# Kernel tuning notes

Hardware: AMD Instinct MI355X
Metric: run time of the kernel (lower is better)

Reference implementation:

```python
import jax, jax.numpy as jnp
import numpy as np

B, S = 512, 256          # batch, seq_len
C, H = 8, 16             # num_cells, expert hidden size
M = 20                   # memory_size (hard-coded in module)
NT = C * H               # num_trajectories = 128
ENC_IN = M * (NT + 1)    # 20*129 = 2580, memory_encode input dim
A_H = 16                 # agent LSTM hidden


def setup_inputs() -> dict:
    key = jax.random.key(0)
    ks = jax.random.split(key, 20)
    r = lambda i, shape: 0.1 * jax.random.normal(ks[i], shape, dtype=jnp.float32)
    return {
        "x": jax.random.normal(ks[0], (B, S, 1), dtype=jnp.float32),
        "pred0": jax.random.uniform(ks[1], (B, 1), dtype=jnp.float32),
        "gate0": jax.nn.softmax(jax.random.uniform(ks[2], (B, C), dtype=jnp.float32), axis=1),
        # experts: C parallel LSTM cells (input 1, hidden H) + per-cell scalar head
        "W_ih": r(3, (C, 4 * H, 1)), "W_hh": r(4, (C, 4 * H, H)),
        "b_ih": r(5, (C, 4 * H)), "b_hh": r(6, (C, 4 * H)),
        "W_o": r(7, (C, H)), "b_o": r(8, (C,)),
        # memory_encode: Linear(2580,64) ReLU Linear(64,16) ReLU
        "W1": r(9, (64, ENC_IN)), "b1": r(10, (64,)),
        "W2": r(11, (16, 64)), "b2": r(12, (16,)),
        # gate_linear: Linear(16, C) + softmax
        "Wg": r(13, (C, 16)), "bg": r(14, (C,)),
        # agent: 2 stacked LSTM cells (16 -> 16)
        "Wa_ih": r(15, (2, 4 * A_H, A_H)), "Wa_hh": r(16, (2, 4 * A_H, A_H)),
        "ba_ih": r(17, (2, 4 * A_H)), "ba_hh": r(18, (2, 4 * A_H)),
    }


def _cell(z, c):
    # PyTorch LSTMCell gate order: i, f, g, o
    i, f, g, o = jnp.split(z, 4, axis=-1)
    c2 = jax.nn.sigmoid(f) * c + jax.nn.sigmoid(i) * jnp.tanh(g)
    return jax.nn.sigmoid(o) * jnp.tanh(c2), c2


def reference(x, pred0, gate0, W_ih, W_hh, b_ih, b_hh, W_o, b_o,
              W1, b1, W2, b2, Wg, bg, Wa_ih, Wa_hh, ba_ih, ba_hh):
    mem0 = jnp.zeros((B, M, NT + 1), jnp.float32).at[:, :, -1].set(0.5)
    eh0 = jnp.zeros((B, H), jnp.float32)   # combined expert h (shared across cells)
    a0 = jnp.zeros((2, B, A_H), jnp.float32)

    def step(carry, x_t):
        mem, eh, ec, pred, gate_state, ah, ac = carry
        error = x_t - pred                                        # [B,1]
        # experts: C LSTM cells, all reading the shared combined state
        z = (jnp.einsum('bf,cgf->bcg', x_t, W_ih)
             + jnp.einsum('bh,cgh->bcg', eh, W_hh)
             + b_ih + b_hh)                                       # [B,C,4H]
        nh, nc = _cell(z, ec[:, None, :])                          # [B,C,H]
        o = jnp.einsum('bch,ch->bc', nh, W_o) + b_o               # [B,C]
        # memory_step: matmul(mstep, mem) shifts rows down by 1, row 0 <- w
        w = jnp.concatenate([nh.reshape(B, -1), error], axis=1)   # [B,NT+1]
        mem = jnp.concatenate([w[:, None, :], mem[:, :-1, :]], axis=1)
        # memory_encode MLP
        e1 = jax.nn.relu(mem.reshape(B, -1) @ W1.T + b1)
        ai = jax.nn.relu(e1 @ W2.T + b2)                           # [B,16]
        # agent: 2 stacked LSTM cells
        ah_l, ac_l, inp_l = [], [], ai
        for l in range(2):
            zl = inp_l @ Wa_ih[l].T + ba_ih[l] + ah[l] @ Wa_hh[l].T + ba_hh[l]
            hl, cl = _cell(zl, ac[l])
            ah_l.append(hl); ac_l.append(cl)
            inp_l = hl
        ah2, ac2 = jnp.stack(ah_l), jnp.stack(ac_l)
        gate = jax.nn.softmax(inp_l @ Wg.T + bg, axis=1)           # [B,C]
        # theta = clip(2.5 * mean|mem[:, :10, -1]|, 0, 1)  (relu(t)-relu(t-1))
        theta = jnp.clip(jnp.mean(jnp.abs(mem[:, :10, -1]), axis=1) * 2.5, 0.0, 1.0)[:, None]
        gate = gate * theta + gate_state * (1.0 - theta)
        eh2 = jnp.einsum('bc,bch->bh', gate, nh)                   # bmm(gate, h)
        ec2 = jnp.einsum('bc,bch->bh', gate, nc)
        pred2 = jnp.einsum('bc,bc->b', gate, o)[:, None]           # [B,1]
        return (mem, eh2, ec2, pred2, gate, ah2, ac2), pred2

    xs = jnp.swapaxes(x, 0, 1)  # [S,B,1]
    _, preds = jax.lax.scan(step, (mem0, eh0, eh0, pred0, gate0, a0, a0), xs)
    return jnp.swapaxes(preds, 0, 1)  # [B,S,1]
```

## Files before the change

kernel.cpp:

```cpp
#include <hip/hip_runtime.h>
#include <math.h>

#define S_LEN 256
#define NCELL 8
#define HID 16
#define MEM 20
#define NB 4
#define NTHR 512
#define RSTR 2592
#define RP 80

typedef _Float16 v8h __attribute__((ext_vector_type(8)));
typedef _Float16 v4h __attribute__((ext_vector_type(4)));
typedef float v4f __attribute__((ext_vector_type(4)));

__device__ __forceinline__ float sigm(float v) { return 1.0f / (1.0f + __expf(-v)); }
__device__ __forceinline__ float tanh_f(float v) { return 1.0f - 2.0f / (__expf(2.0f * v) + 1.0f); }
__device__ __forceinline__ float dot4(float4 a, float4 b) {
    return fmaf(a.x, b.x, fmaf(a.y, b.y, fmaf(a.z, b.z, a.w * b.w)));
}
__device__ __forceinline__ v4f mfma16(v8h a, v8h b, v4f c) {
    return __builtin_amdgcn_mfma_f32_16x16x32_f16(a, b, c, 0, 0, 0);
}

#define RING(b, s, k) ringH[(b) * RSTR + (s) * 128 + (k)]

__global__ __launch_bounds__(256)
void prep_w(const float* __restrict__ W1, const float* __restrict__ W_hh,
            const float* __restrict__ W_ih, const float* __restrict__ b_ih,
            const float* __restrict__ b_hh, const float* __restrict__ W2,
            const float* __restrict__ Wa_ih, const float* __restrict__ Wa_hh,
            _Float16* __restrict__ W1F, _Float16* __restrict__ WAF,
            _Float16* __restrict__ W2F, _Float16* __restrict__ WAGF) {
    int idx = blockIdx.x * 256 + threadIdx.x;
    if (idx < 163840) {
        int e = idx & 7, lane = (idx >> 3) & 63, jt = (idx >> 9) & 3, t = idx >> 11;
        int m = t >> 2, kc = t & 3;
        int j = jt * 16 + (lane & 15);
        int k = kc * 32 + (lane >> 4) * 8 + e;
        W1F[idx] = (_Float16)W1[j * 2580 + m * 129 + k];
    } else if (idx < 163840 + 16384) {
        int d = idx - 163840;
        int e = d & 7, lane = (d >> 3) & 63, gate = (d >> 9) & 3, c = d >> 11;
        int m = lane & 15, k = (lane >> 4) * 8 + e;
        int row = c * 64 + gate * 16 + m;
        float v = 0.f;
        if (k < 16) v = W_hh[row * 16 + k];
        else if (k == 16) v = W_ih[row];
        else if (k == 17) v = b_ih[row] + b_hh[row];
        WAF[d] = (_Float16)v;
    } else if (idx < 163840 + 16384 + 1024) {
        int d = idx - 163840 - 16384;
        int e = d & 7, lane = (d >> 3) & 63, kc = d >> 9;
        int i = lane & 15, k = kc * 32 + (lane >> 4) * 8 + e;
        W2F[d] = (_Float16)W2[i * 64 + k];
    } else if (idx < 163840 + 16384 + 1024 + 4096) {
        int d = idx - 163840 - 16384 - 1024;
        int e = d & 7, lane = (d >> 3) & 63, jt = (d >> 9) & 3, l = d >> 11;
        int g = jt * 16 + (lane & 15);
        int k = (lane >> 4) * 8 + e;
        float v = (k < 16) ? Wa_ih[(l * 64 + g) * 16 + k]
                           : Wa_hh[(l * 64 + g) * 16 + (k - 16)];
        WAGF[d] = (_Float16)v;
    }
}

#define E1P(BB, V) { \
    V = b1_l[lane] \
      + red[par][1][BB][lane] + red[par][2][BB][lane] + red[par][3][BB][lane] \
      + red[par][4][BB][lane] + red[par][5][BB][lane] + red[par][6][BB][lane] \
      + red[par][7][BB][lane]; }

__global__ __attribute__((amdgpu_flat_work_group_size(NTHR, NTHR)))
void mmoe_kernel(const float* __restrict__ x, const float* __restrict__ pred0,
                 const float* __restrict__ gate0,
                 const float* __restrict__ W_ih, const float* __restrict__ W_hh,
                 const float* __restrict__ b_ih, const float* __restrict__ b_hh,
                 const float* __restrict__ W_o, const float* __restrict__ b_o,
                 const float* __restrict__ W1, const float* __restrict__ b1,
                 const float* __restrict__ W2, const float* __restrict__ b2,
                 const float* __restrict__ Wg, const float* __restrict__ bg,
                 const float* __restrict__ Wa_ih, const float* __restrict__ Wa_hh,
                 const float* __restrict__ ba_ih, const float* __restrict__ ba_hh,
                 const _Float16* __restrict__ W1F, const _Float16* __restrict__ WAF,
                 const _Float16* __restrict__ W2F, const _Float16* __restrict__ WAGF,
                 float* __restrict__ out)
{
    __shared__ __align__(16) _Float16 ringH[NB * RSTR];
    __shared__ __align__(16) _Float16 ehH[NB][40];
    __shared__ __align__(16) _Float16 W2F_l[2 * 512];
    __shared__ __align__(16) _Float16 WaG_l[2 * 4 * 512];
    __shared__ __align__(16) _Float16 e1B[NB][64];
    __shared__ __align__(16) _Float16 agB0[NB][32];
    __shared__ __align__(16) _Float16 agB1[NB][32];
    __shared__ float errS[NB][MEM];
    __shared__ float ba_l[2][64];
    __shared__ float b2_l[16];
    __shared__ __align__(16) float Wg_l[8][16], Wo_l[8][16];
    __shared__ float bg_l[8], bo_l[8];
    __shared__ float Werr_l[MEM * 64];
    __shared__ float b1_l[64];
    __shared__ float xS[NB][S_LEN];
    __shared__ __align__(16) float ecS[NB][HID];
    __shared__ __align__(16) float nhS[NCELL][NB][HID];
    __shared__ __align__(16) float ncS[NCELL][NB][HID];
    __shared__ float oS[NB][NCELL], predS[NB], gateS[NB][NCELL];
    __shared__ __align__(16) float acS[2][NB][HID];
    __shared__ __align__(16) float ah1S[NB][HID];
    __shared__ __align__(16) float glog[NB][8];
    __shared__ __align__(16) float red[2][8][NB][RP];
    __shared__ __align__(16) float red0[4][NB][RP];
    __shared__ float errdotS[NB][64];
    __shared__ float thS[NB];

    const int tid = threadIdx.x;
    const int b0 = blockIdx.x * NB;
    const int lane = tid & 63, wv = tid >> 6;
    const int quad = lane >> 4, nn = lane & 15, bb4 = nn & 3;

    for (int i = tid; i < 128; i += NTHR) { int l = i >> 6, g = i & 63; ba_l[l][g] = ba_ih[i] + ba_hh[i]; }
    for (int i = tid; i < 1024; i += NTHR) W2F_l[i] = W2F[i];
    for (int i = tid; i < 4096; i += NTHR) WaG_l[i] = WAGF[i];
    for (int i = tid; i < 1280; i += NTHR) { int m = i >> 6, j = i & 63; Werr_l[i] = W1[j * 2580 + m * 129 + 128]; }
    if (tid < 64) b1_l[tid] = b1[tid];
    if (tid < 16) b2_l[tid] = b2[tid];
    if (tid < 128) { int c = tid >> 4, h = tid & 15; Wg_l[c][h] = Wg[tid]; Wo_l[c][h] = W_o[tid]; }
    if (tid < 8) { bg_l[tid] = bg[tid]; bo_l[tid] = b_o[tid]; }
    for (int i = tid; i < NB * S_LEN; i += NTHR) { int b = i >> 8, s = i & 255; xS[b][s] = x[(b0 + b) * S_LEN + s]; }
    for (int i = tid; i < NB * RSTR; i += NTHR) ringH[i] = (_Float16)0.0f;
    for (int i = tid; i < 2 * 8 * NB * RP; i += NTHR) ((float*)red)[i] = 0.0f;
    for (int i = tid; i < NB * 32; i += NTHR) { ((_Float16*)agB0)[i] = (_Float16)0.0f; ((_Float16*)agB1)[i] = (_Float16)0.0f; }
    if (tid < NB * 40) {
        int n = tid / 40, k = tid % 40;
        float v = 0.f;
        if (k == 16) v = x[(b0 + n) * S_LEN + 0];
        else if (k == 17) v = 1.0f;
        ehH[n][k] = (_Float16)v;
    }
    if (tid < NB * MEM) { int b = tid / MEM, m = tid % MEM; errS[b][m] = 0.5f; }
    if (tid < NB * HID) {
        int b = tid >> 4, h = tid & 15;
        ecS[b][h] = 0.f;
        acS[0][b][h] = 0.f; acS[1][b][h] = 0.f;
        ah1S[b][h] = 0.f;
    }
    if (tid < NB) predS[tid] = pred0[b0 + tid];
    if (tid < NB * NCELL) { int b = tid >> 3, c = tid & 7; gateS[b][c] = gate0[(b0 + b) * NCELL + c]; }

    const v8h* WA = (const v8h*)WAF;
    v8h aI = WA[(wv * 4 + 0) * 64 + lane];
    v8h aF = WA[(wv * 4 + 1) * 64 + lane];
    v8h aG = WA[(wv * 4 + 2) * 64 + lane];
    v8h aO = WA[(wv * 4 + 3) * 64 + lane];
    const v8h* Wb = (const v8h*)W1F;
    const int kcW = wv >> 1, jt0W = (wv & 1) * 2;
    v8h m0A = Wb[(size_t)(kcW * 4 + jt0W) * 64 + lane];
    v8h m0B = Wb[(size_t)(kcW * 4 + jt0W + 1) * 64 + lane];
    const v8h* W2Fv = (const v8h*)W2F_l;
    const v8h* WaGv = (const v8h*)WaG_l;
    __syncthreads();
    v4f b2v;
    #pragma unroll
    for (int r = 0; r < 4; ++r) b2v[r] = b2_l[quad * 4 + r];

    int head = 0;
    #pragma unroll 1
    for (int t = 0; t < S_LEN; ++t) {
        head = (head == 0) ? (MEM - 1) : (head - 1);
        const int par = t & 1, np = par ^ 1;
        float v0, v1, v2, v3;

        {
            v8h bfrag = *(const v8h*)&ehH[bb4][quad * 8];
            v4f z4 = {0.f, 0.f, 0.f, 0.f};
            v4f zi = mfma16(aI, bfrag, z4);
            v4f zf = mfma16(aF, bfrag, z4);
            v4f zg = mfma16(aG, bfrag, z4);
            v4f zo = mfma16(aO, bfrag, z4);
            if (nn < 4) {
                int b = nn, c = wv;
                v4f hv4, cv4; v4h hr;
                #pragma unroll
                for (int r = 0; r < 4; ++r) {
                    int h = quad * 4 + r;
                    float cc = ecS[b][h];
                    float c2 = sigm(zf[r]) * cc + sigm(zi[r]) * tanh_f(zg[r]);
                    float hv = sigm(zo[r]) * tanh_f(c2);
                    hv4[r] = hv; cv4[r] = c2; hr[r] = (_Float16)hv;
                }
                *(v4f*)&nhS[c][b][quad * 4] = hv4;
                *(v4f*)&ncS[c][b][quad * 4] = cv4;
                *(v4h*)&RING(b, head, c * 16 + quad * 4) = hr;
            }
            if (tid < NB) errS[tid][head] = xS[tid][t] - predS[tid];
        }
        __syncthreads();

        {
            v8h bfrag = *(const v8h*)&RING(bb4, head, kcW * 32 + quad * 8);
            v4f z = {0.f, 0.f, 0.f, 0.f};
            v4f c0 = mfma16(m0A, bfrag, z);
            v4f c1 = mfma16(m0B, bfrag, z);
            if (nn < 4) {
                *(v4f*)&red0[kcW][nn][jt0W * 16 + quad * 4] = c0;
                *(v4f*)&red0[kcW][nn][(jt0W + 1) * 16 + quad * 4] = c1;
            }
            if (wv == 0) {
                E1P(0, v0) E1P(1, v1) E1P(2, v2) E1P(3, v3)
            } else if (wv == 1) {
                if (lane < 32) {
                    int bb = lane >> 3, c = lane & 7;
                    const float4* np_ = (const float4*)&nhS[c][bb][0];
                    const float4* wp = (const float4*)&Wo_l[c][0];
                    float s = bo_l[c];
                    #pragma unroll
                    for (int q4 = 0; q4 < 4; ++q4) s += dot4(np_[q4], wp[q4]);
                    oS[bb][c] = s;
                }
            } else if (wv == 2) {
                if (lane < NB) {
                    float th = 0.f;
                    #pragma unroll
                    for (int m = 0; m < 10; ++m) {
                        int sl = head + m; if (sl >= MEM) sl -= MEM;
                        th += fabsf(errS[lane][sl]);
                    }
                    th *= 0.25f;
                    thS[lane] = fminf(fmaxf(th, 0.f), 1.f);
                }
            } else if (wv >= 3 && wv < 7) {
                int bb = wv - 3;
                float s = 0.f;
                int sl = head;
                #pragma unroll
                for (int m = 0; m < MEM; ++m) {
                    s = fmaf(Werr_l[m * 64 + lane], errS[bb][sl], s);
                    ++sl; if (sl >= MEM) sl = 0;
                }
                errdotS[bb][lane] = s;
            }
        }
        __syncthreads();

        if (wv >= 1) {
            int kt = (wv - 1) * 11;
            int ktEnd = kt + 11; if (ktEnd > 76) ktEnd = 76;
            v4f c0 = {0.f,0.f,0.f,0.f}, c1 = {0.f,0.f,0.f,0.f};
            v4f c2 = {0.f,0.f,0.f,0.f}, c3 = {0.f,0.f,0.f,0.f};
            size_t tb = (size_t)(4 + kt) * 256 + lane;
            v8h pA0 = Wb[tb], pA1 = Wb[tb + 64], pA2 = Wb[tb + 128], pA3 = Wb[tb + 192];
            int m0 = 1 + (kt >> 2), kc0 = kt & 3;
            int s0 = head + m0 - 1; if (s0 >= MEM) s0 -= MEM;
            v8h pB = *(const v8h*)&RING(bb4, s0, kc0 * 32 + quad * 8);
            #pragma unroll 1
            for (; kt < ktEnd; ++kt) {
                v8h A0 = pA0, A1 = pA1, A2 = pA2, A3 = pA3, B = pB;
                int kn = kt + 1;
                if (kn < ktEnd) {
                    size_t tn = (size_t)(4 + kn) * 256 + lane;
                    pA0 = Wb[tn]; pA1 = Wb[tn + 64]; pA2 = Wb[tn + 128]; pA3 = Wb[tn + 192];
                    int mn = 1 + (kn >> 2), kcn = kn & 3;
                    int sn = head + mn - 1; if (sn >= MEM) sn -= MEM;
                    pB = *(const v8h*)&RING(bb4, sn, kcn * 32 + quad * 8);
                }
                c0 = mfma16(A0, B, c0);
                c1 = mfma16(A1, B, c1);
                c2 = mfma16(A2, B, c2);
                c3 = mfma16(A3, B, c3);
            }
            if (nn < 4) {
                *(v4f*)&red[np][wv][nn][ 0 + quad * 4] = c0;
                *(v4f*)&red[np][wv][nn][16 + quad * 4] = c1;
                *(v4f*)&red[np][wv][nn][32 + quad * 4] = c2;
                *(v4f*)&red[np][wv][nn][48 + quad * 4] = c3;
            }
        } else {
            {
                float r0 = fmaxf(v0 + errdotS[0][lane]
                       + red0[0][0][lane] + red0[1][0][lane] + red0[2][0][lane] + red0[3][0][lane], 0.f);
                float r1 = fmaxf(v1 + errdotS[1][lane]
                       + red0[0][1][lane] + red0[1][1][lane] + red0[2][1][lane] + red0[3][1][lane], 0.f);
                float r2 = fmaxf(v2 + errdotS[2][lane]
                       + red0[0][2][lane] + red0[1][2][lane] + red0[2][2][lane] + red0[3][2][lane], 0.f);
                float r3 = fmaxf(v3 + errdotS[3][lane]
                       + red0[0][3][lane] + red0[1][3][lane] + red0[2][3][lane] + red0[3][3][lane], 0.f);
                e1B[0][lane] = (_Float16)r0;
                e1B[1][lane] = (_Float16)r1;
                e1B[2][lane] = (_Float16)r2;
                e1B[3][lane] = (_Float16)r3;
            }
            {
                v8h bk0 = *(const v8h*)&e1B[bb4][quad * 8];
                v8h bk1 = *(const v8h*)&e1B[bb4][32 + quad * 8];
                v4f cai = mfma16(W2Fv[lane], bk0, b2v);
                cai = mfma16(W2Fv[64 + lane], bk1, cai);
                if (nn < 4) {
                    v4h av;
                    #pragma unroll
                    for (int r = 0; r < 4; ++r) av[r] = (_Float16)fmaxf(cai[r], 0.f);
                    *(v4h*)&agB0[nn][quad * 4] = av;
                }
            }
            {
                v8h bf = *(const v8h*)&agB0[bb4][quad * 8];
                v4f z4 = {0.f, 0.f, 0.f, 0.f};
                v4f zi = mfma16(WaGv[0 * 64 + lane], bf, z4);
                v4f zf = mfma16(WaGv[1 * 64 + lane], bf, z4);
                v4f zg = mfma16(WaGv[2 * 64 + lane], bf, z4);
                v4f zo = mfma16(WaGv[3 * 64 + lane], bf, z4);
                if (nn < 4) {
                    v4h hr;
                    #pragma unroll
                    for (int r = 0; r < 4; ++r) {
                        int g = quad * 4 + r;
                        float zi_ = zi[r] + ba_l[0][g], zf_ = zf[r] + ba_l[0][16 + g];
                        float zg_ = zg[r] + ba_l[0][32 + g], zo_ = zo[r] + ba_l[0][48 + g];
                        float c2 = sigm(zf_) * acS[0][nn][g] + sigm(zi_) * tanh_f(zg_);
                        acS[0][nn][g] = c2;
                        hr[r] = (_Float16)(sigm(zo_) * tanh_f(c2));
                    }
                    *(v4h*)&agB1[nn][quad * 4] = hr;
                    *(v4h*)&agB0[nn][16 + quad * 4] = hr;
                }
            }
            {
                v8h bf = *(const v8h*)&agB1[bb4][quad * 8];
                v4f z4 = {0.f, 0.f, 0.f, 0.f};
                v4f zi = mfma16(WaGv[4 * 64 + lane], bf, z4);
                v4f zf = mfma16(WaGv[5 * 64 + lane], bf, z4);
                v4f zg = mfma16(WaGv[6 * 64 + lane], bf, z4);
                v4f zo = mfma16(WaGv[7 * 64 + lane], bf, z4);
                if (nn < 4) {
                    v4h hr; v4f hf;
                    #pragma unroll
                    for (int r = 0; r < 4; ++r) {
                        int g = quad * 4 + r;
                        float zi_ = zi[r] + ba_l[1][g], zf_ = zf[r] + ba_l[1][16 + g];
                        float zg_ = zg[r] + ba_l[1][32 + g], zo_ = zo[r] + ba_l[1][48 + g];
                        float c2 = sigm(zf_) * acS[1][nn][g] + sigm(zi_) * tanh_f(zg_);
                        acS[1][nn][g] = c2;
                        float hv = sigm(zo_) * tanh_f(c2);
                        hf[r] = hv; hr[r] = (_Float16)hv;
                    }
                    *(v4f*)&ah1S[nn][quad * 4] = hf;
                    *(v4h*)&agB1[nn][16 + quad * 4] = hr;
                }
            }
            const int j = lane;
            if (j < 32) {
                int bb = j >> 3, c = j & 7;
                const float4* hp = (const float4*)&ah1S[bb][0];
                const float4* wg = (const float4*)&Wg_l[c][0];
                float s = bg_l[c];
                #pragma unroll
                for (int q = 0; q < 4; ++q) s += dot4(wg[q], hp[q]);
                glog[bb][c] = s;
                float4 ga = *(const float4*)&glog[bb][0];
                float4 gb = *(const float4*)&glog[bb][4];
                float mx = fmaxf(fmaxf(fmaxf(ga.x, ga.y), fmaxf(ga.z, ga.w)),
                                 fmaxf(fmaxf(gb.x, gb.y), fmaxf(gb.z, gb.w)));
                float sum = __expf(ga.x - mx) + __expf(ga.y - mx) + __expf(ga.z - mx) + __expf(ga.w - mx)
                          + __expf(gb.x - mx) + __expf(gb.y - mx) + __expf(gb.z - mx) + __expf(gb.w - mx);
                float p = __expf(s - mx) / sum;
                float th = thS[bb];
                gateS[bb][c] = p * th + gateS[bb][c] * (1.f - th);
            }
            {
                int bb = j >> 4, h = j & 15;
                float se = 0.f, sc = 0.f;
                #pragma unroll
                for (int c = 0; c < 8; ++c) {
                    float g = gateS[bb][c];
                    se = fmaf(g, nhS[c][bb][h], se);
                    sc = fmaf(g, ncS[c][bb][h], sc);
                }
                ehH[bb][h] = (_Float16)se;
                ecS[bb][h] = sc;
            }
            if (j < NB) {
                float s = 0.f;
                #pragma unroll
                for (int c = 0; c < 8; ++c) s = fmaf(gateS[j][c], oS[j][c], s);
                predS[j] = s;
                out[(b0 + j) * S_LEN + t] = s;
                ehH[j][16] = (_Float16)((t + 1 < S_LEN) ? xS[j][t + 1] : 0.f);
            }
        }
        __syncthreads();
    }
}

extern "C" void kernel_launch(void* const* d_in, const int* in_sizes, int n_in,
                              void* d_out, int out_size, void* d_ws, size_t ws_size,
                              hipStream_t stream) {
    const float* xp    = (const float*)d_in[0];
    const float* pred0 = (const float*)d_in[1];
    const float* gate0 = (const float*)d_in[2];
    const float* W_ih  = (const float*)d_in[3];
    const float* W_hh  = (const float*)d_in[4];
    const float* b_ih  = (const float*)d_in[5];
    const float* b_hh  = (const float*)d_in[6];
    const float* W_o   = (const float*)d_in[7];
    const float* b_o   = (const float*)d_in[8];
    const float* W1    = (const float*)d_in[9];
    const float* b1    = (const float*)d_in[10];
    const float* W2    = (const float*)d_in[11];
    const float* b2    = (const float*)d_in[12];
    const float* Wg    = (const float*)d_in[13];
    const float* bg    = (const float*)d_in[14];
    const float* Wa_ih = (const float*)d_in[15];
    const float* Wa_hh = (const float*)d_in[16];
    const float* ba_ih = (const float*)d_in[17];
    const float* ba_hh = (const float*)d_in[18];
    _Float16* W1F  = (_Float16*)d_ws;
    _Float16* WAF  = W1F + 163840;
    _Float16* W2F  = WAF + 16384;
    _Float16* WAGF = W2F + 1024;

    prep_w<<<(163840 + 16384 + 1024 + 4096 + 255) / 256, 256, 0, stream>>>(
        W1, W_hh, W_ih, b_ih, b_hh, W2, Wa_ih, Wa_hh, W1F, WAF, W2F, WAGF);
    mmoe_kernel<<<512 / NB, NTHR, 0, stream>>>(
        xp, pred0, gate0, W_ih, W_hh, b_ih, b_hh, W_o, b_o,
        W1, b1, W2, b2, Wg, bg, Wa_ih, Wa_hh, ba_ih, ba_hh,
        W1F, WAF, W2F, WAGF, (float*)d_out);
}
```

Measured before the change: 1.268 ms.

## Keep agent LSTM and gate state in registers, exchange via ds_bpermute

```diff
diff --git a/kernel.cpp b/kernel.cpp
--- a/kernel.cpp
+++ b/kernel.cpp
@@ -13,6 +13,8 @@
 typedef _Float16 v8h __attribute__((ext_vector_type(8)));
 typedef _Float16 v4h __attribute__((ext_vector_type(4)));
 typedef float v4f __attribute__((ext_vector_type(4)));
+typedef int v2i __attribute__((ext_vector_type(2)));
+typedef int v4i __attribute__((ext_vector_type(4)));
 
 __device__ __forceinline__ float sigm(float v) { return 1.0f / (1.0f + __expf(-v)); }
 __device__ __forceinline__ float tanh_f(float v) { return 1.0f - 2.0f / (__expf(2.0f * v) + 1.0f); }
@@ -21,6 +23,9 @@
 }
 __device__ __forceinline__ v4f mfma16(v8h a, v8h b, v4f c) {
     return __builtin_amdgcn_mfma_f32_16x16x32_f16(a, b, c, 0, 0, 0);
+}
+__device__ __forceinline__ int bperm(int idx4, int v) {
+    return __builtin_amdgcn_ds_bpermute(idx4, v);
 }
 
 #define RING(b, s, k) ringH[(b) * RSTR + (s) * 128 + (k)]
@@ -91,10 +96,8 @@
     __shared__ __align__(16) _Float16 W2F_l[2 * 512];
     __shared__ __align__(16) _Float16 WaG_l[2 * 4 * 512];
     __shared__ __align__(16) _Float16 e1B[NB][64];
-    __shared__ __align__(16) _Float16 agB0[NB][32];
-    __shared__ __align__(16) _Float16 agB1[NB][32];
     __shared__ float errS[NB][MEM];
-    __shared__ float ba_l[2][64];
+    __shared__ __align__(16) float ba_l[2][64];
     __shared__ float b2_l[16];
     __shared__ __align__(16) float Wg_l[8][16], Wo_l[8][16];
     __shared__ float bg_l[8], bo_l[8];
@@ -104,10 +107,8 @@
     __shared__ __align__(16) float ecS[NB][HID];
     __shared__ __align__(16) float nhS[NCELL][NB][HID];
     __shared__ __align__(16) float ncS[NCELL][NB][HID];
-    __shared__ float oS[NB][NCELL], predS[NB], gateS[NB][NCELL];
-    __shared__ __align__(16) float acS[2][NB][HID];
-    __shared__ __align__(16) float ah1S[NB][HID];
-    __shared__ __align__(16) float glog[NB][8];
+    __shared__ __align__(16) float oS[NB][NCELL];
+    __shared__ float predS[NB];
     __shared__ __align__(16) float red[2][8][NB][RP];
     __shared__ __align__(16) float red0[4][NB][RP];
     __shared__ float errdotS[NB][64];
@@ -129,7 +130,6 @@
     for (int i = tid; i < NB * S_LEN; i += NTHR) { int b = i >> 8, s = i & 255; xS[b][s] = x[(b0 + b) * S_LEN + s]; }
     for (int i = tid; i < NB * RSTR; i += NTHR) ringH[i] = (_Float16)0.0f;
     for (int i = tid; i < 2 * 8 * NB * RP; i += NTHR) ((float*)red)[i] = 0.0f;
-    for (int i = tid; i < NB * 32; i += NTHR) { ((_Float16*)agB0)[i] = (_Float16)0.0f; ((_Float16*)agB1)[i] = (_Float16)0.0f; }
     if (tid < NB * 40) {
         int n = tid / 40, k = tid % 40;
         float v = 0.f;
@@ -138,14 +138,15 @@
         ehH[n][k] = (_Float16)v;
     }
     if (tid < NB * MEM) { int b = tid / MEM, m = tid % MEM; errS[b][m] = 0.5f; }
-    if (tid < NB * HID) {
-        int b = tid >> 4, h = tid & 15;
-        ecS[b][h] = 0.f;
-        acS[0][b][h] = 0.f; acS[1][b][h] = 0.f;
-        ah1S[b][h] = 0.f;
-    }
+    if (tid < NB * HID) { int b = tid >> 4, h = tid & 15; ecS[b][h] = 0.f; }
     if (tid < NB) predS[tid] = pred0[b0 + tid];
-    if (tid < NB * NCELL) { int b = tid >> 3, c = tid & 7; gateS[b][c] = gate0[(b0 + b) * NCELL + c]; }
+
+    float gS0 = gate0[(b0 + bb4) * NCELL + 0], gS1 = gate0[(b0 + bb4) * NCELL + 1];
+    float gS2 = gate0[(b0 + bb4) * NCELL + 2], gS3 = gate0[(b0 + bb4) * NCELL + 3];
+    float gS4 = gate0[(b0 + bb4) * NCELL + 4], gS5 = gate0[(b0 + bb4) * NCELL + 5];
+    float gS6 = gate0[(b0 + bb4) * NCELL + 6], gS7 = gate0[(b0 + bb4) * NCELL + 7];
+    v4f ac0 = {0.f, 0.f, 0.f, 0.f}, ac1 = {0.f, 0.f, 0.f, 0.f};
+    v2i h0p = {0, 0}, h1p = {0, 0};
 
     const v8h* WA = (const v8h*)WAF;
     v8h aI = WA[(wv * 4 + 0) * 64 + lane];
@@ -171,26 +172,24 @@
         float v0, v1, v2, v3;
 
         {
+            v4f ecv = *(const v4f*)&ecS[bb4][quad * 4];
             v8h bfrag = *(const v8h*)&ehH[bb4][quad * 8];
             v4f z4 = {0.f, 0.f, 0.f, 0.f};
             v4f zi = mfma16(aI, bfrag, z4);
             v4f zf = mfma16(aF, bfrag, z4);
             v4f zg = mfma16(aG, bfrag, z4);
             v4f zo = mfma16(aO, bfrag, z4);
+            v4f hv4, cv4; v4h hrS;
+            #pragma unroll
+            for (int r = 0; r < 4; ++r) {
+                float c2 = sigm(zf[r]) * ecv[r] + sigm(zi[r]) * tanh_f(zg[r]);
+                float hv = sigm(zo[r]) * tanh_f(c2);
+                hv4[r] = hv; cv4[r] = c2; hrS[r] = (_Float16)hv;
+            }
             if (nn < 4) {
-                int b = nn, c = wv;
-                v4f hv4, cv4; v4h hr;
-                #pragma unroll
-                for (int r = 0; r < 4; ++r) {
-                    int h = quad * 4 + r;
-                    float cc = ecS[b][h];
-                    float c2 = sigm(zf[r]) * cc + sigm(zi[r]) * tanh_f(zg[r]);
-                    float hv = sigm(zo[r]) * tanh_f(c2);
-                    hv4[r] = hv; cv4[r] = c2; hr[r] = (_Float16)hv;
-                }
-                *(v4f*)&nhS[c][b][quad * 4] = hv4;
-                *(v4f*)&ncS[c][b][quad * 4] = cv4;
-                *(v4h*)&RING(b, head, c * 16 + quad * 4) = hr;
+                *(v4f*)&nhS[wv][nn][quad * 4] = hv4;
+                *(v4f*)&ncS[wv][nn][quad * 4] = cv4;
+                *(v4h*)&RING(nn, head, wv * 16 + quad * 4) = hrS;
             }
             if (tid < NB) errS[tid][head] = xS[tid][t] - predS[tid];
         }
@@ -275,6 +274,16 @@
                 *(v4f*)&red[np][wv][nn][48 + quad * 4] = c3;
             }
         } else {
+            v8h w2a = W2Fv[lane], w2b = W2Fv[64 + lane];
+            v8h agA0 = WaGv[0 * 64 + lane], agA1 = WaGv[1 * 64 + lane];
+            v8h agA2 = WaGv[2 * 64 + lane], agA3 = WaGv[3 * 64 + lane];
+            v4f bI0 = *(const v4f*)&ba_l[0][ 0 + quad * 4];
+            v4f bF0 = *(const v4f*)&ba_l[0][16 + quad * 4];
+            v4f bG0 = *(const v4f*)&ba_l[0][32 + quad * 4];
+            v4f bO0 = *(const v4f*)&ba_l[0][48 + quad * 4];
+            float theta = thS[bb4];
+            v4f oA = *(const v4f*)&oS[bb4][0], oB = *(const v4f*)&oS[bb4][4];
+
             {
                 float r0 = fmaxf(v0 + errdotS[0][lane]
                        + red0[0][0][lane] + red0[1][0][lane] + red0[2][0][lane] + red0[3][0][lane], 0.f);
@@ -289,101 +298,154 @@
                 e1B[2][lane] = (_Float16)r2;
                 e1B[3][lane] = (_Float16)r3;
             }
+            v8h bk0 = *(const v8h*)&e1B[bb4][quad * 8];
+            v8h bk1 = *(const v8h*)&e1B[bb4][32 + quad * 8];
+            v4f z4 = {0.f, 0.f, 0.f, 0.f};
+            v4f cai = mfma16(w2a, bk0, b2v);
+            cai = mfma16(w2b, bk1, cai);
+            v4h av;
+            #pragma unroll
+            for (int r = 0; r < 4; ++r) av[r] = (_Float16)fmaxf(cai[r], 0.f);
+
+            const int idxA4 = (nn + ((quad & 1) << 5)) << 2;
+            const int idxB4 = idxA4 + 64;
+            const bool lowq = (quad < 2);
+
+            v2i avd = __builtin_bit_cast(v2i, av);
+            int tiA0 = bperm(idxA4, avd.x), tiA1 = bperm(idxA4, avd.y);
+            int tiB0 = bperm(idxB4, avd.x), tiB1 = bperm(idxB4, avd.y);
+            int thA0 = bperm(idxA4, h0p.x), thA1 = bperm(idxA4, h0p.y);
+            int thB0 = bperm(idxB4, h0p.x), thB1 = bperm(idxB4, h0p.y);
+            v4i wB0;
+            wB0[0] = lowq ? tiA0 : thA0;
+            wB0[1] = lowq ? tiA1 : thA1;
+            wB0[2] = lowq ? tiB0 : thB0;
+            wB0[3] = lowq ? tiB1 : thB1;
+            v8h bf0 = __builtin_bit_cast(v8h, wB0);
+            v4f zi = mfma16(agA0, bf0, z4);
+            v4f zf = mfma16(agA1, bf0, z4);
+            v4f zg = mfma16(agA2, bf0, z4);
+            v4f zo = mfma16(agA3, bf0, z4);
+            v8h agA4 = WaGv[4 * 64 + lane], agA5 = WaGv[5 * 64 + lane];
+            v8h agA6 = WaGv[6 * 64 + lane], agA7 = WaGv[7 * 64 + lane];
+            v4f bI1 = *(const v4f*)&ba_l[1][ 0 + quad * 4];
+            v4f bF1 = *(const v4f*)&ba_l[1][16 + quad * 4];
+            v4f bG1 = *(const v4f*)&ba_l[1][32 + quad * 4];
+            v4f bO1 = *(const v4f*)&ba_l[1][48 + quad * 4];
+            const int cbb = lane >> 4, chh = lane & 15;
+            float nhp0 = nhS[0][cbb][chh], nhp1 = nhS[1][cbb][chh];
+            float nhp2 = nhS[2][cbb][chh], nhp3 = nhS[3][cbb][chh];
+            float nhp4 = nhS[4][cbb][chh], nhp5 = nhS[5][cbb][chh];
+            float nhp6 = nhS[6][cbb][chh], nhp7 = nhS[7][cbb][chh];
+            float ncp0 = ncS[0][cbb][chh], ncp1 = ncS[1][cbb][chh];
+            float ncp2 = ncS[2][cbb][chh], ncp3 = ncS[3][cbb][chh];
+            float ncp4 = ncS[4][cbb][chh], ncp5 = ncS[5][cbb][chh];
+            float ncp6 = ncS[6][cbb][chh], ncp7 = ncS[7][cbb][chh];
+            v4f wg0 = *(const v4f*)&Wg_l[0][quad * 4], wg1 = *(const v4f*)&Wg_l[1][quad * 4];
+            v4f wg2 = *(const v4f*)&Wg_l[2][quad * 4], wg3 = *(const v4f*)&Wg_l[3][quad * 4];
+            v4f wg4 = *(const v4f*)&Wg_l[4][quad * 4], wg5 = *(const v4f*)&Wg_l[5][quad * 4];
+            v4f wg6 = *(const v4f*)&Wg_l[6][quad * 4], wg7 = *(const v4f*)&Wg_l[7][quad * 4];
+            float bg0 = bg_l[0], bg1 = bg_l[1], bg2 = bg_l[2], bg3 = bg_l[3];
+            float bg4 = bg_l[4], bg5 = bg_l[5], bg6 = bg_l[6], bg7 = bg_l[7];
+            v4h hr0;
+            #pragma unroll
+            for (int r = 0; r < 4; ++r) {
+                float zi_ = zi[r] + bI0[r], zf_ = zf[r] + bF0[r];
+                float zg_ = zg[r] + bG0[r], zo_ = zo[r] + bO0[r];
+                float c2 = sigm(zf_) * ac0[r] + sigm(zi_) * tanh_f(zg_);
+                ac0[r] = c2;
+                hr0[r] = (_Float16)(sigm(zo_) * tanh_f(c2));
+            }
+            v2i h0n = __builtin_bit_cast(v2i, hr0);
+
+            int uiA0 = bperm(idxA4, h0n.x), uiA1 = bperm(idxA4, h0n.y);
+            int uiB0 = bperm(idxB4, h0n.x), uiB1 = bperm(idxB4, h0n.y);
+            int uhA0 = bperm(idxA4, h1p.x), uhA1 = bperm(idxA4, h1p.y);
+            int uhB0 = bperm(idxB4, h1p.x), uhB1 = bperm(idxB4, h1p.y);
+            v4i wB1;
+            wB1[0] = lowq ? uiA0 : uhA0;
+            wB1[1] = lowq ? uiA1 : uhA1;
+            wB1[2] = lowq ? uiB0 : uhB0;
+            wB1[3] = lowq ? uiB1 : uhB1;
+            v8h bf1 = __builtin_bit_cast(v8h, wB1);
+            v4f yi = mfma16(agA4, bf1, z4);
+            v4f yf = mfma16(agA5, bf1, z4);
+            v4f yg = mfma16(agA6, bf1, z4);
+            v4f yo = mfma16(agA7, bf1, z4);
+            h0p = h0n;
+            v4h hr1; v4f hf;
+            #pragma unroll
+            for (int r = 0; r < 4; ++r) {
+                float yi_ = yi[r] + bI1[r], yf_ = yf[r] + bF1[r];
+                float yg_ = yg[r] + bG1[r], yo_ = yo[r] + bO1[r];
+                float c2 = sigm(yf_) * ac1[r] + sigm(yi_) * tanh_f(yg_);
+                ac1[r] = c2;
+                float hv = sigm(yo_) * tanh_f(c2);
+                hf[r] = hv; hr1[r] = (_Float16)hv;
+            }
+            h1p = __builtin_bit_cast(v2i, hr1);
+
+            float p0 = wg0[0]*hf[0] + wg0[1]*hf[1] + wg0[2]*hf[2] + wg0[3]*hf[3];
+            float p1 = wg1[0]*hf[0] + wg1[1]*hf[1] + wg1[2]*hf[2] + wg1[3]*hf[3];
+            float p2 = wg2[0]*hf[0] + wg2[1]*hf[1] + wg2[2]*hf[2] + wg2[3]*hf[3];
+            float p3 = wg3[0]*hf[0] + wg3[1]*hf[1] + wg3[2]*hf[2] + wg3[3]*hf[3];
+            float p4 = wg4[0]*hf[0] + wg4[1]*hf[1] + wg4[2]*hf[2] + wg4[3]*hf[3];
+            float p5 = wg5[0]*hf[0] + wg5[1]*hf[1] + wg5[2]*hf[2] + wg5[3]*hf[3];
+            float p6 = wg6[0]*hf[0] + wg6[1]*hf[1] + wg6[2]*hf[2] + wg6[3]*hf[3];
+            float p7 = wg7[0]*hf[0] + wg7[1]*hf[1] + wg7[2]*hf[2] + wg7[3]*hf[3];
+            p0 += __shfl_xor(p0, 16); p0 += __shfl_xor(p0, 32);
+            p1 += __shfl_xor(p1, 16); p1 += __shfl_xor(p1, 32);
+            p2 += __shfl_xor(p2, 16); p2 += __shfl_xor(p2, 32);
+            p3 += __shfl_xor(p3, 16); p3 += __shfl_xor(p3, 32);
+            p4 += __shfl_xor(p4, 16); p4 += __shfl_xor(p4, 32);
+            p5 += __shfl_xor(p5, 16); p5 += __shfl_xor(p5, 32);
+            p6 += __shfl_xor(p6, 16); p6 += __shfl_xor(p6, 32);
+            p7 += __shfl_xor(p7, 16); p7 += __shfl_xor(p7, 32);
+            p0 += bg0; p1 += bg1; p2 += bg2; p3 += bg3;
+            p4 += bg4; p5 += bg5; p6 += bg6; p7 += bg7;
+            float mx = fmaxf(fmaxf(fmaxf(p0, p1), fmaxf(p2, p3)),
+                             fmaxf(fmaxf(p4, p5), fmaxf(p6, p7)));
+            float e0 = __expf(p0 - mx), e1 = __expf(p1 - mx), e2 = __expf(p2 - mx), e3 = __expf(p3 - mx);
+            float e4 = __expf(p4 - mx), e5 = __expf(p5 - mx), e6 = __expf(p6 - mx), e7 = __expf(p7 - mx);
+            float sum = ((e0 + e1) + (e2 + e3)) + ((e4 + e5) + (e6 + e7));
+            float inv = 1.0f / sum;
+            float omt = 1.f - theta;
+            gS0 = e0 * inv * theta + gS0 * omt;
+            gS1 = e1 * inv * theta + gS1 * omt;
+            gS2 = e2 * inv * theta + gS2 * omt;
+            gS3 = e3 * inv * theta + gS3 * omt;
+            gS4 = e4 * inv * theta + gS4 * omt;
+            gS5 = e5 * inv * theta + gS5 * omt;
+            gS6 = e6 * inv * theta + gS6 * omt;
+            gS7 = e7 * inv * theta + gS7 * omt;
+
             {
-                v8h bk0 = *(const v8h*)&e1B[bb4][quad * 8];
-                v8h bk1 = *(const v8h*)&e1B[bb4][32 + quad * 8];
-                v4f cai = mfma16(W2Fv[lane], bk0, b2v);
-                cai = mfma16(W2Fv[64 + lane], bk1, cai);
-                if (nn < 4) {
-                    v4h av;
-                    #pragma unroll
-                    for (int r = 0; r < 4; ++r) av[r] = (_Float16)fmaxf(cai[r], 0.f);
-                    *(v4h*)&agB0[nn][quad * 4] = av;
-                }
-            }
-            {
-                v8h bf = *(const v8h*)&agB0[bb4][quad * 8];
-                v4f z4 = {0.f, 0.f, 0.f, 0.f};
-                v4f zi = mfma16(WaGv[0 * 64 + lane], bf, z4);
-                v4f zf = mfma16(WaGv[1 * 64 + lane], bf, z4);
-                v4f zg = mfma16(WaGv[2 * 64 + lane], bf, z4);
-                v4f zo = mfma16(WaGv[3 * 64 + lane], bf, z4);
-                if (nn < 4) {
-                    v4h hr;
-                    #pragma unroll
-                    for (int r = 0; r < 4; ++r) {
-                        int g = quad * 4 + r;
-                        float zi_ = zi[r] + ba_l[0][g], zf_ = zf[r] + ba_l[0][16 + g];
-                        float zg_ = zg[r] + ba_l[0][32 + g], zo_ = zo[r] + ba_l[0][48 + g];
-                        float c2 = sigm(zf_) * acS[0][nn][g] + sigm(zi_) * tanh_f(zg_);
-                        acS[0][nn][g] = c2;
-                        hr[r] = (_Float16)(sigm(zo_) * tanh_f(c2));
-                    }
-                    *(v4h*)&agB1[nn][quad * 4] = hr;
-                    *(v4h*)&agB0[nn][16 + quad * 4] = hr;
-                }
-            }
-            {
-                v8h bf = *(const v8h*)&agB1[bb4][quad * 8];
-                v4f z4 = {0.f, 0.f, 0.f, 0.f};
-                v4f zi = mfma16(WaGv[4 * 64 + lane], bf, z4);
-                v4f zf = mfma16(WaGv[5 * 64 + lane], bf, z4);
-                v4f zg = mfma16(WaGv[6 * 64 + lane], bf, z4);
-                v4f zo = mfma16(WaGv[7 * 64 + lane], bf, z4);
-                if (nn < 4) {
-                    v4h hr; v4f hf;
-                    #pragma unroll
-                    for (int r = 0; r < 4; ++r) {
-                        int g = quad * 4 + r;
-                        float zi_ = zi[r] + ba_l[1][g], zf_ = zf[r] + ba_l[1][16 + g];
-                        float zg_ = zg[r] + ba_l[1][32 + g], zo_ = zo[r] + ba_l[1][48 + g];
-                        float c2 = sigm(zf_) * acS[1][nn][g] + sigm(zi_) * tanh_f(zg_);
-                        acS[1][nn][g] = c2;
-                        float hv = sigm(zo_) * tanh_f(c2);
-                        hf[r] = hv; hr[r] = (_Float16)hv;
-                    }
-                    *(v4f*)&ah1S[nn][quad * 4] = hf;
-                    *(v4h*)&agB1[nn][16 + quad * 4] = hr;
-                }
-            }
-            const int j = lane;
-            if (j < 32) {
-                int bb = j >> 3, c = j & 7;
-                const float4* hp = (const float4*)&ah1S[bb][0];
-                const float4* wg = (const float4*)&Wg_l[c][0];
-                float s = bg_l[c];
-                #pragma unroll
-                for (int q = 0; q < 4; ++q) s += dot4(wg[q], hp[q]);
-                glog[bb][c] = s;
-                float4 ga = *(const float4*)&glog[bb][0];
-                float4 gb = *(const float4*)&glog[bb][4];
-                float mx = fmaxf(fmaxf(fmaxf(ga.x, ga.y), fmaxf(ga.z, ga.w)),
-                                 fmaxf(fmaxf(gb.x, gb.y), fmaxf(gb.z, gb.w)));
-                float sum = __expf(ga.x - mx) + __expf(ga.y - mx) + __expf(ga.z - mx) + __expf(ga.w - mx)
-                          + __expf(gb.x - mx) + __expf(gb.y - mx) + __expf(gb.z - mx) + __expf(gb.w - mx);
-                float p = __expf(s - mx) / sum;
-                float th = thS[bb];
-                gateS[bb][c] = p * th + gateS[bb][c] * (1.f - th);
-            }
-            {
-                int bb = j >> 4, h = j & 15;
-                float se = 0.f, sc = 0.f;
-                #pragma unroll
-                for (int c = 0; c < 8; ++c) {
-                    float g = gateS[bb][c];
-                    se = fmaf(g, nhS[c][bb][h], se);
-                    sc = fmaf(g, ncS[c][bb][h], sc);
-                }
-                ehH[bb][h] = (_Float16)se;
-                ecS[bb][h] = sc;
-            }
-            if (j < NB) {
-                float s = 0.f;
-                #pragma unroll
-                for (int c = 0; c < 8; ++c) s = fmaf(gateS[j][c], oS[j][c], s);
-                predS[j] = s;
-                out[(b0 + j) * S_LEN + t] = s;
-                ehH[j][16] = (_Float16)((t + 1 < S_LEN) ? xS[j][t + 1] : 0.f);
+                const int gi = cbb << 2;
+                float g0 = __int_as_float(bperm(gi, __float_as_int(gS0)));
+                float g1 = __int_as_float(bperm(gi, __float_as_int(gS1)));
+                float g2 = __int_as_float(bperm(gi, __float_as_int(gS2)));
+                float g3 = __int_as_float(bperm(gi, __float_as_int(gS3)));
+                float g4 = __int_as_float(bperm(gi, __float_as_int(gS4)));
+                float g5 = __int_as_float(bperm(gi, __float_as_int(gS5)));
+                float g6 = __int_as_float(bperm(gi, __float_as_int(gS6)));
+                float g7 = __int_as_float(bperm(gi, __float_as_int(gS7)));
+                float se = g0 * nhp0, sc = g0 * ncp0;
+                se = fmaf(g1, nhp1, se); sc = fmaf(g1, ncp1, sc);
+                se = fmaf(g2, nhp2, se); sc = fmaf(g2, ncp2, sc);
+                se = fmaf(g3, nhp3, se); sc = fmaf(g3, ncp3, sc);
+                se = fmaf(g4, nhp4, se); sc = fmaf(g4, ncp4, sc);
+                se = fmaf(g5, nhp5, se); sc = fmaf(g5, ncp5, sc);
+                se = fmaf(g6, nhp6, se); sc = fmaf(g6, ncp6, sc);
+                se = fmaf(g7, nhp7, se); sc = fmaf(g7, ncp7, sc);
+                ehH[cbb][chh] = (_Float16)se;
+                ecS[cbb][chh] = sc;
+            }
+            if (lane < 4) {
+                float s = gS0 * oA[0] + gS1 * oA[1] + gS2 * oA[2] + gS3 * oA[3]
+                        + gS4 * oB[0] + gS5 * oB[1] + gS6 * oB[2] + gS7 * oB[3];
+                predS[lane] = s;
+                out[(b0 + lane) * S_LEN + t] = s;
+                ehH[lane][16] = (_Float16)((t + 1 < S_LEN) ? xS[lane][t + 1] : 0.f);
             }
         }
         __syncthreads();
```

Measured after the change: 1.270 ms. About the same (+0.1%).
